# Kernel optimization log

Measured on AMD Instinct MI355X. Metric: run time of the kernel, lower is better.

Reference implementation:

```python
import jax, jax.numpy as jnp
import numpy as np

N_NODES = 10000
N_EDGES = 640000
NF = 128
HID = 128
NORM_FACTOR = 100.0


def setup_inputs() -> dict:
    key = jax.random.key(0)
    ks = jax.random.split(key, 8)
    s = lambda fan_in: 1.0 / np.sqrt(fan_in)
    return {
        "h": jax.random.normal(ks[0], (N_NODES, NF), dtype=jnp.float32),
        "edge_index": jax.random.randint(ks[1], (2, N_EDGES), 0, N_NODES, dtype=jnp.int64),
        "ew1": jax.random.normal(ks[2], (2 * NF, HID), dtype=jnp.float32) * s(2 * NF),
        "eb1": jnp.zeros((HID,), dtype=jnp.float32),
        "ew2": jax.random.normal(ks[3], (HID, HID), dtype=jnp.float32) * s(HID),
        "eb2": jnp.zeros((HID,), dtype=jnp.float32),
        "nw1": jax.random.normal(ks[4], (HID + NF, HID), dtype=jnp.float32) * s(HID + NF),
        "nb1": jnp.zeros((HID,), dtype=jnp.float32),
        "nw2": jax.random.normal(ks[5], (HID, NF), dtype=jnp.float32) * s(HID),
        "nb2": jnp.zeros((NF,), dtype=jnp.float32),
    }


def reference(h, edge_index, ew1, eb1, ew2, eb2, nw1, nb1, nw2, nb2):
    row, col = edge_index[0], edge_index[1]
    # edge model: gather endpoints, concat, 2-layer SiLU MLP -> mij [E, HID]
    x = jnp.concatenate([h[row], h[col]], axis=1)          # [E, 2*NF]
    mij = jax.nn.silu(x @ ew1 + eb1)
    mij = jax.nn.silu(mij @ ew2 + eb2)                     # [E, HID]
    # aggregation: scatter-add messages to source nodes, 'sum' normalization
    agg = jax.ops.segment_sum(mij, row, num_segments=h.shape[0]) / NORM_FACTOR
    # node model: residual MLP update
    a = jnp.concatenate([h, agg], axis=1)                  # [V, NF+HID]
    out = h + (jax.nn.silu(a @ nw1 + nb1) @ nw2 + nb2)     # [V, NF]
    return out, mij
```

## Files before the change

### kernel.cpp

```cpp
#include <hip/hip_runtime.h>

typedef __attribute__((ext_vector_type(8))) short short8;
typedef __attribute__((ext_vector_type(4))) float f32x4;
typedef unsigned short ushort_t;
typedef unsigned int uint_t;

#define MFMA16(a, b, c) __builtin_amdgcn_mfma_f32_16x16x32_bf16((a), (b), (c), 0, 0, 0)

constexpr int V = 10000;
constexpr int E = 640000;

__device__ __forceinline__ ushort_t f2b(float f) {
    uint_t u = __float_as_uint(f);
    u += 0x7FFFu + ((u >> 16) & 1u);
    return (ushort_t)(u >> 16);
}

__device__ __forceinline__ float silu(float x) {
    return x / (1.0f + __expf(-x));
}

__device__ __forceinline__ uint_t cvt_pk_bf16(float lo, float hi) {
    uint_t r;
    asm("v_cvt_pk_bf16_f32 %0, %1, %2" : "=v"(r) : "v"(lo), "v"(hi));
    return r;
}

__device__ __forceinline__ void wg_barrier_lds() {
    asm volatile("s_waitcnt lgkmcnt(0)" ::: "memory");
    __builtin_amdgcn_s_barrier();
    asm volatile("" ::: "memory");
}

__global__ void prep(const float* __restrict__ h,
                     const float* __restrict__ ew1, const float* __restrict__ ew2,
                     const float* __restrict__ nw1, const float* __restrict__ nw2,
                     ushort_t* __restrict__ hb,
                     ushort_t* __restrict__ w1T, ushort_t* __restrict__ w2T,
                     ushort_t* __restrict__ nw1T, ushort_t* __restrict__ nw2T,
                     float* __restrict__ agg) {
    int i = blockIdx.x * blockDim.x + threadIdx.x;
    if (i < V * 128) { hb[i] = f2b(h[i]); return; }
    i -= V * 128;
    if (i < V * 128) { agg[i] = 0.0f; return; }
    i -= V * 128;
    if (i < 256 * 128) { int k = i >> 7, c = i & 127; w1T[c * 256 + k] = f2b(ew1[i]); return; }
    i -= 256 * 128;
    if (i < 128 * 128) { int k = i >> 7, c = i & 127; w2T[c * 128 + k] = f2b(ew2[i]); return; }
    i -= 128 * 128;
    if (i < 256 * 128) { int k = i >> 7, c = i & 127; nw1T[c * 256 + k] = f2b(nw1[i]); return; }
    i -= 256 * 128;
    if (i < 128 * 128) { int k = i >> 7, c = i & 127; nw2T[c * 128 + k] = f2b(nw2[i]); }
}

__global__ __launch_bounds__(256, 2) void edge_kernel(
    const ushort_t* __restrict__ hb, const int* __restrict__ eidx,
    const ushort_t* __restrict__ w1, const float* __restrict__ eb1,
    const ushort_t* __restrict__ w2, const float* __restrict__ eb2,
    float* __restrict__ mij, float* __restrict__ agg) {
    __shared__ __align__(16) ushort_t xs[64 * 256];
    __shared__ __align__(16) ushort_t ys[64 * 128];
    __shared__ int ridx[2][64];

    const int tid = threadIdx.x;
    const int wave = tid >> 6;
    const int lane = tid & 63;
    const int quad = lane >> 4;
    const int ln = lane & 15;
    const int ncol0 = wave * 32;

    short8 b1f[8][2];
    short8 b2f[4][2];
#pragma unroll
    for (int kk = 0; kk < 8; kk++)
#pragma unroll
        for (int t = 0; t < 2; t++)
            b1f[kk][t] = *(const short8*)(w1 + (ncol0 + t * 16 + ln) * 256 + kk * 32 + quad * 8);
#pragma unroll
    for (int kk = 0; kk < 4; kk++)
#pragma unroll
        for (int t = 0; t < 2; t++)
            b2f[kk][t] = *(const short8*)(w2 + (ncol0 + t * 16 + ln) * 128 + kk * 32 + quad * 8);
    const float bv1[2] = {eb1[ncol0 + ln], eb1[ncol0 + 16 + ln]};
    const float bv2[2] = {eb2[ncol0 + ln], eb2[ncol0 + 16 + ln]};

    const int NT = E / 64;
    const int e = lane;
    const int seg = wave;
    char* const xrow = (char*)xs + e * 512;
    const int xswz = (e & 7) << 4;

    int tile = blockIdx.x;

    {
        const int r = eidx[tile * 64 + e];
        const int c = eidx[E + tile * 64 + e];
        if (seg == 0) ridx[0][e] = r;
        const int node = (seg < 2) ? r : c;
        const uint4* src = (const uint4*)(hb + node * 128 + (seg & 1) * 64);
#pragma unroll
        for (int u = 0; u < 8; u++)
            *(uint4*)(xrow + ((seg * 128 + u * 16) ^ xswz)) = src[u];
    }
    wg_barrier_lds();

    int p = 0;
    for (; tile < NT; tile += gridDim.x) {
        const int e0 = tile * 64;
        int tn = tile + gridDim.x;
        if (tn >= NT) tn = tile;

        const int rn = eidx[tn * 64 + e];
        const int cn = eidx[E + tn * 64 + e];
        const int noden = (seg < 2) ? rn : cn;
        const uint4* srcn = (const uint4*)(hb + noden * 128 + (seg & 1) * 64);
        uint4 st[8];
#pragma unroll
        for (int u = 0; u < 8; u++) st[u] = srcn[u];

        f32x4 acc[4][2];
#pragma unroll
        for (int mt = 0; mt < 4; mt++)
#pragma unroll
            for (int t = 0; t < 2; t++) acc[mt][t] = f32x4{bv1[t], bv1[t], bv1[t], bv1[t]};
#pragma unroll
        for (int kk = 0; kk < 8; kk++)
#pragma unroll
            for (int mt = 0; mt < 4; mt++) {
                const int row = mt * 16 + ln;
                short8 a = *(const short8*)((char*)xs + row * 512 +
                                            ((kk * 64 + quad * 16) ^ ((ln & 7) << 4)));
                acc[mt][0] = MFMA16(a, b1f[kk][0], acc[mt][0]);
                acc[mt][1] = MFMA16(a, b1f[kk][1], acc[mt][1]);
            }
#pragma unroll
        for (int mt = 0; mt < 4; mt++)
#pragma unroll
            for (int r4 = 0; r4 < 4; r4++) {
                const int row = mt * 16 + quad * 4 + r4;
                const uint_t pk = cvt_pk_bf16(silu(acc[mt][0][r4]), silu(acc[mt][1][r4]));
                char* yrow = (char*)ys + row * 256;
                const int ysw = (row & 7) << 4;
                const int cb = 2 * (ncol0 + ln);
                *(ushort_t*)(yrow + (cb ^ ysw)) = (ushort_t)pk;
                *(ushort_t*)(yrow + ((cb + 32) ^ ysw)) = (ushort_t)(pk >> 16);
            }
        wg_barrier_lds();

        if (seg == 0) ridx[p ^ 1][e] = rn;
#pragma unroll
        for (int u = 0; u < 8; u++)
            *(uint4*)(xrow + ((seg * 128 + u * 16) ^ xswz)) = st[u];

        f32x4 acc2[4][2];
#pragma unroll
        for (int mt = 0; mt < 4; mt++)
#pragma unroll
            for (int t = 0; t < 2; t++) acc2[mt][t] = f32x4{bv2[t], bv2[t], bv2[t], bv2[t]};
#pragma unroll
        for (int kk = 0; kk < 4; kk++)
#pragma unroll
            for (int mt = 0; mt < 4; mt++) {
                const int row = mt * 16 + ln;
                short8 a = *(const short8*)((char*)ys + row * 256 +
                                            ((kk * 64 + quad * 16) ^ ((ln & 7) << 4)));
                acc2[mt][0] = MFMA16(a, b2f[kk][0], acc2[mt][0]);
                acc2[mt][1] = MFMA16(a, b2f[kk][1], acc2[mt][1]);
            }

#pragma unroll
        for (int mt = 0; mt < 4; mt++)
#pragma unroll
            for (int r4 = 0; r4 < 4; r4++) {
                const int row = mt * 16 + quad * 4 + r4;
                const int nsrc = ridx[p][row];
#pragma unroll
                for (int t = 0; t < 2; t++) {
                    const float s = silu(acc2[mt][t][r4]);
                    const int col = ncol0 + t * 16 + ln;
                    mij[(size_t)(e0 + row) * 128 + col] = s;
                    unsafeAtomicAdd(&agg[nsrc * 128 + col], s);
                }
            }
        wg_barrier_lds();
        p ^= 1;
    }
}

__global__ __launch_bounds__(256, 2) void node_kernel(
    const ushort_t* __restrict__ hb, const float* __restrict__ h32,
    const float* __restrict__ agg,
    const ushort_t* __restrict__ w1, const float* __restrict__ nb1,
    const ushort_t* __restrict__ w2, const float* __restrict__ nb2,
    float* __restrict__ out) {
    __shared__ __align__(16) ushort_t xs[64 * 256];
    __shared__ __align__(16) ushort_t ys[64 * 128];

    const int tid = threadIdx.x;
    const int wave = tid >> 6;
    const int lane = tid & 63;
    const int quad = lane >> 4;
    const int ln = lane & 15;
    const int ncol0 = wave * 32;
    const int i0 = blockIdx.x * 64;

    short8 b1f[8][2];
    short8 b2f[4][2];
#pragma unroll
    for (int kk = 0; kk < 8; kk++)
#pragma unroll
        for (int t = 0; t < 2; t++)
            b1f[kk][t] = *(const short8*)(w1 + (ncol0 + t * 16 + ln) * 256 + kk * 32 + quad * 8);
#pragma unroll
    for (int kk = 0; kk < 4; kk++)
#pragma unroll
        for (int t = 0; t < 2; t++)
            b2f[kk][t] = *(const short8*)(w2 + (ncol0 + t * 16 + ln) * 128 + kk * 32 + quad * 8);
    const float bv1[2] = {nb1[ncol0 + ln], nb1[ncol0 + 16 + ln]};
    const float bv2[2] = {nb2[ncol0 + ln], nb2[ncol0 + 16 + ln]};

    const int e = lane, seg = wave;
    char* const xrow = (char*)xs + e * 512;
    const int xswz = (e & 7) << 4;
    const int node = i0 + e;

    if (node < V) {
        if (seg < 2) {
            const uint4* src = (const uint4*)(hb + node * 128 + seg * 64);
#pragma unroll
            for (int u = 0; u < 8; u++)
                *(uint4*)(xrow + ((seg * 128 + u * 16) ^ xswz)) = src[u];
        } else {
            const float4* src = (const float4*)(agg + node * 128 + (seg & 1) * 64);
#pragma unroll
            for (int u = 0; u < 8; u++) {
                float4 a = src[2 * u], b = src[2 * u + 1];
                uint4 v;
                v.x = cvt_pk_bf16(a.x * 0.01f, a.y * 0.01f);
                v.y = cvt_pk_bf16(a.z * 0.01f, a.w * 0.01f);
                v.z = cvt_pk_bf16(b.x * 0.01f, b.y * 0.01f);
                v.w = cvt_pk_bf16(b.z * 0.01f, b.w * 0.01f);
                *(uint4*)(xrow + ((seg * 128 + u * 16) ^ xswz)) = v;
            }
        }
    } else {
        const uint4 z{0, 0, 0, 0};
#pragma unroll
        for (int u = 0; u < 8; u++)
            *(uint4*)(xrow + ((seg * 128 + u * 16) ^ xswz)) = z;
    }
    __syncthreads();

    f32x4 acc[4][2];
#pragma unroll
    for (int mt = 0; mt < 4; mt++)
#pragma unroll
        for (int t = 0; t < 2; t++) acc[mt][t] = f32x4{bv1[t], bv1[t], bv1[t], bv1[t]};
#pragma unroll
    for (int kk = 0; kk < 8; kk++)
#pragma unroll
        for (int mt = 0; mt < 4; mt++) {
            const int row = mt * 16 + ln;
            short8 a = *(const short8*)((char*)xs + row * 512 +
                                        ((kk * 64 + quad * 16) ^ ((ln & 7) << 4)));
            acc[mt][0] = MFMA16(a, b1f[kk][0], acc[mt][0]);
            acc[mt][1] = MFMA16(a, b1f[kk][1], acc[mt][1]);
        }
#pragma unroll
    for (int mt = 0; mt < 4; mt++)
#pragma unroll
        for (int r4 = 0; r4 < 4; r4++) {
            const int row = mt * 16 + quad * 4 + r4;
            const uint_t pk = cvt_pk_bf16(silu(acc[mt][0][r4]), silu(acc[mt][1][r4]));
            char* yrow = (char*)ys + row * 256;
            const int ysw = (row & 7) << 4;
            const int cb = 2 * (ncol0 + ln);
            *(ushort_t*)(yrow + (cb ^ ysw)) = (ushort_t)pk;
            *(ushort_t*)(yrow + ((cb + 32) ^ ysw)) = (ushort_t)(pk >> 16);
        }
    __syncthreads();

    f32x4 acc2[4][2];
#pragma unroll
    for (int mt = 0; mt < 4; mt++)
#pragma unroll
        for (int t = 0; t < 2; t++) acc2[mt][t] = f32x4{bv2[t], bv2[t], bv2[t], bv2[t]};
#pragma unroll
    for (int kk = 0; kk < 4; kk++)
#pragma unroll
        for (int mt = 0; mt < 4; mt++) {
            const int row = mt * 16 + ln;
            short8 a = *(const short8*)((char*)ys + row * 256 +
                                        ((kk * 64 + quad * 16) ^ ((ln & 7) << 4)));
            acc2[mt][0] = MFMA16(a, b2f[kk][0], acc2[mt][0]);
            acc2[mt][1] = MFMA16(a, b2f[kk][1], acc2[mt][1]);
        }
#pragma unroll
    for (int mt = 0; mt < 4; mt++)
#pragma unroll
        for (int r4 = 0; r4 < 4; r4++) {
            const int row = mt * 16 + quad * 4 + r4;
            const int nd = i0 + row;
            if (nd < V) {
#pragma unroll
                for (int t = 0; t < 2; t++) {
                    const int col = ncol0 + t * 16 + ln;
                    out[(size_t)nd * 128 + col] = h32[(size_t)nd * 128 + col] + acc2[mt][t][r4];
                }
            }
        }
}

extern "C" void kernel_launch(void* const* d_in, const int* in_sizes, int n_in,
                              void* d_out, int out_size, void* d_ws, size_t ws_size,
                              hipStream_t stream) {
    const float* h = (const float*)d_in[0];
    const int* eidx = (const int*)d_in[1];
    const float* ew1 = (const float*)d_in[2];
    const float* eb1 = (const float*)d_in[3];
    const float* ew2 = (const float*)d_in[4];
    const float* eb2 = (const float*)d_in[5];
    const float* nw1 = (const float*)d_in[6];
    const float* nb1 = (const float*)d_in[7];
    const float* nw2 = (const float*)d_in[8];
    const float* nb2 = (const float*)d_in[9];

    float* out = (float*)d_out;
    float* mij = (float*)d_out + (size_t)V * 128;

    uint8_t* ws = (uint8_t*)d_ws;
    ushort_t* hb = (ushort_t*)(ws);
    ushort_t* w1b = (ushort_t*)(ws + 2560000);
    ushort_t* w2b = (ushort_t*)(ws + 2560000 + 65536);
    ushort_t* nw1b = (ushort_t*)(ws + 2560000 + 98304);
    ushort_t* nw2b = (ushort_t*)(ws + 2560000 + 163840);
    float* agg = (float*)(ws + 2560000 + 196608);

    constexpr int PREP_N = V * 128 + V * 128 + 256 * 128 + 128 * 128 + 256 * 128 + 128 * 128;
    prep<<<(PREP_N + 255) / 256, 256, 0, stream>>>(h, ew1, ew2, nw1, nw2,
                                                   hb, w1b, w2b, nw1b, nw2b, agg);

    edge_kernel<<<2000, 256, 0, stream>>>(hb, eidx, w1b, eb1, w2b, eb2, mij, agg);
    node_kernel<<<(V + 63) / 64, 256, 0, stream>>>(hb, h, agg, nw1b, nb1, nw2b, nb2, out);
}
```

Before: 604.5 us.

## Sort edges by source node and segment-reduce messages before atomics

Adds a counting sort (histogram, single-block scan, scatter) that builds a permutation of edges grouped by source node. The edge kernel processes edges in that order, writes mij at the original edge index, and sums each run of equal source nodes within the tile using ballot and shuffles. Each run then issues one atomic per column instead of one per edge. This targets the heavy global atomic traffic on agg, at the cost of extra preprocessing kernels, indirect index loads and a per-segment masked reduction loop.

```diff
diff --git a/kernel.cpp b/kernel.cpp
--- a/kernel.cpp
+++ b/kernel.cpp
@@ -38,7 +38,7 @@
                      ushort_t* __restrict__ hb,
                      ushort_t* __restrict__ w1T, ushort_t* __restrict__ w2T,
                      ushort_t* __restrict__ nw1T, ushort_t* __restrict__ nw2T,
-                     float* __restrict__ agg) {
+                     float* __restrict__ agg, int* __restrict__ cnt) {
     int i = blockIdx.x * blockDim.x + threadIdx.x;
     if (i < V * 128) { hb[i] = f2b(h[i]); return; }
     i -= V * 128;
@@ -50,17 +50,65 @@
     i -= 128 * 128;
     if (i < 256 * 128) { int k = i >> 7, c = i & 127; nw1T[c * 256 + k] = f2b(nw1[i]); return; }
     i -= 256 * 128;
-    if (i < 128 * 128) { int k = i >> 7, c = i & 127; nw2T[c * 128 + k] = f2b(nw2[i]); }
+    if (i < 128 * 128) { int k = i >> 7, c = i & 127; nw2T[c * 128 + k] = f2b(nw2[i]); return; }
+    i -= 128 * 128;
+    if (i < V) cnt[i] = 0;
+}
+
+__global__ void hist_kernel(const int* __restrict__ eidx, int* __restrict__ cnt) {
+    int e = blockIdx.x * blockDim.x + threadIdx.x;
+    if (e < E) atomicAdd(&cnt[eidx[e]], 1);
+}
+
+__global__ __launch_bounds__(256) void scan_kernel(const int* __restrict__ cnt,
+                                                   int* __restrict__ cursor) {
+    __shared__ int part[256];
+    const int t = threadIdx.x;
+    const int base = t * 40;
+    int s = 0;
+#pragma unroll 1
+    for (int i = 0; i < 40; i++) {
+        int idx = base + i;
+        s += (idx < V) ? cnt[idx] : 0;
+    }
+    part[t] = s;
+    __syncthreads();
+    for (int off = 1; off < 256; off <<= 1) {
+        int v = (t >= off) ? part[t - off] : 0;
+        __syncthreads();
+        part[t] += v;
+        __syncthreads();
+    }
+    int run = (t == 0) ? 0 : part[t - 1];
+#pragma unroll 1
+    for (int i = 0; i < 40; i++) {
+        int idx = base + i;
+        if (idx < V) {
+            cursor[idx] = run;
+            run += cnt[idx];
+        }
+    }
+}
+
+__global__ void scatter_kernel(const int* __restrict__ eidx, int* __restrict__ cursor,
+                               int* __restrict__ perm) {
+    int e = blockIdx.x * blockDim.x + threadIdx.x;
+    if (e < E) {
+        int pos = atomicAdd(&cursor[eidx[e]], 1);
+        perm[pos] = e;
+    }
 }
 
 __global__ __launch_bounds__(256, 2) void edge_kernel(
     const ushort_t* __restrict__ hb, const int* __restrict__ eidx,
+    const int* __restrict__ perm,
     const ushort_t* __restrict__ w1, const float* __restrict__ eb1,
     const ushort_t* __restrict__ w2, const float* __restrict__ eb2,
     float* __restrict__ mij, float* __restrict__ agg) {
     __shared__ __align__(16) ushort_t xs[64 * 256];
     __shared__ __align__(16) ushort_t ys[64 * 128];
     __shared__ int ridx[2][64];
+    __shared__ int pidx[2][64];
 
     const int tid = threadIdx.x;
     const int wave = tid >> 6;
@@ -68,6 +116,7 @@
     const int quad = lane >> 4;
     const int ln = lane & 15;
     const int ncol0 = wave * 32;
+    const int lnswz = (ln & 7) << 4;
 
     short8 b1f[8][2];
     short8 b2f[4][2];
@@ -85,6 +134,7 @@
     const float bv2[2] = {eb2[ncol0 + ln], eb2[ncol0 + 16 + ln]};
 
     const int NT = E / 64;
+    const int G = gridDim.x;
     const int e = lane;
     const int seg = wave;
     char* const xrow = (char*)xs + e * 512;
@@ -93,30 +143,34 @@
     int tile = blockIdx.x;
 
     {
-        const int r = eidx[tile * 64 + e];
-        const int c = eidx[E + tile * 64 + e];
-        if (seg == 0) ridx[0][e] = r;
+        const int pe = perm[tile * 64 + e];
+        const int r = eidx[pe];
+        const int c = eidx[E + pe];
+        if (seg == 0) { ridx[0][e] = r; pidx[0][e] = pe; }
         const int node = (seg < 2) ? r : c;
         const uint4* src = (const uint4*)(hb + node * 128 + (seg & 1) * 64);
 #pragma unroll
         for (int u = 0; u < 8; u++)
             *(uint4*)(xrow + ((seg * 128 + u * 16) ^ xswz)) = src[u];
     }
+    int t1 = tile + G; if (t1 >= NT) t1 = tile;
+    int pe1 = perm[t1 * 64 + e];
+    int r1 = eidx[pe1];
+    int c1 = eidx[E + pe1];
     wg_barrier_lds();
 
     int p = 0;
-    for (; tile < NT; tile += gridDim.x) {
-        const int e0 = tile * 64;
-        int tn = tile + gridDim.x;
-        if (tn >= NT) tn = tile;
-
-        const int rn = eidx[tn * 64 + e];
-        const int cn = eidx[E + tn * 64 + e];
-        const int noden = (seg < 2) ? rn : cn;
+    for (; tile < NT; tile += G) {
+        const int noden = (seg < 2) ? r1 : c1;
         const uint4* srcn = (const uint4*)(hb + noden * 128 + (seg & 1) * 64);
         uint4 st[8];
 #pragma unroll
         for (int u = 0; u < 8; u++) st[u] = srcn[u];
+
+        int t2 = tile + 2 * G; if (t2 >= NT) t2 = tile;
+        const int pe2 = perm[t2 * 64 + e];
+        const int r2 = eidx[pe2];
+        const int c2 = eidx[E + pe2];
 
         f32x4 acc[4][2];
 #pragma unroll
@@ -129,7 +183,7 @@
             for (int mt = 0; mt < 4; mt++) {
                 const int row = mt * 16 + ln;
                 short8 a = *(const short8*)((char*)xs + row * 512 +
-                                            ((kk * 64 + quad * 16) ^ ((ln & 7) << 4)));
+                                            ((kk * 64 + quad * 16) ^ lnswz));
                 acc[mt][0] = MFMA16(a, b1f[kk][0], acc[mt][0]);
                 acc[mt][1] = MFMA16(a, b1f[kk][1], acc[mt][1]);
             }
@@ -147,7 +201,7 @@
             }
         wg_barrier_lds();
 
-        if (seg == 0) ridx[p ^ 1][e] = rn;
+        if (seg == 0) { ridx[p ^ 1][e] = r1; pidx[p ^ 1][e] = pe1; }
 #pragma unroll
         for (int u = 0; u < 8; u++)
             *(uint4*)(xrow + ((seg * 128 + u * 16) ^ xswz)) = st[u];
@@ -163,7 +217,7 @@
             for (int mt = 0; mt < 4; mt++) {
                 const int row = mt * 16 + ln;
                 short8 a = *(const short8*)((char*)ys + row * 256 +
-                                            ((kk * 64 + quad * 16) ^ ((ln & 7) << 4)));
+                                            ((kk * 64 + quad * 16) ^ lnswz));
                 acc2[mt][0] = MFMA16(a, b2f[kk][0], acc2[mt][0]);
                 acc2[mt][1] = MFMA16(a, b2f[kk][1], acc2[mt][1]);
             }
@@ -173,16 +227,46 @@
 #pragma unroll
             for (int r4 = 0; r4 < 4; r4++) {
                 const int row = mt * 16 + quad * 4 + r4;
-                const int nsrc = ridx[p][row];
+                const int pe = pidx[p][row];
 #pragma unroll
                 for (int t = 0; t < 2; t++) {
                     const float s = silu(acc2[mt][t][r4]);
-                    const int col = ncol0 + t * 16 + ln;
-                    mij[(size_t)(e0 + row) * 128 + col] = s;
-                    unsafeAtomicAdd(&agg[nsrc * 128 + col], s);
+                    acc2[mt][t][r4] = s;
+                    mij[(size_t)pe * 128 + ncol0 + t * 16 + ln] = s;
                 }
             }
+
+        {
+            const int myn = ridx[p][lane];
+            const int prevn = (lane == 0) ? (myn + 1) : ridx[p][lane - 1];
+            unsigned long long bmask = __ballot(lane == 0 || myn != prevn);
+            while (bmask) {
+                const int a = __builtin_ctzll(bmask);
+                bmask &= bmask - 1;
+                const int b = bmask ? __builtin_ctzll(bmask) : 64;
+                float s0 = 0.0f, s1 = 0.0f;
+#pragma unroll
+                for (int mt = 0; mt < 4; mt++)
+#pragma unroll
+                    for (int r4 = 0; r4 < 4; r4++) {
+                        const int row = mt * 16 + quad * 4 + r4;
+                        const bool in = (row >= a) && (row < b);
+                        s0 += in ? acc2[mt][0][r4] : 0.0f;
+                        s1 += in ? acc2[mt][1][r4] : 0.0f;
+                    }
+                s0 += __shfl_xor(s0, 16);
+                s0 += __shfl_xor(s0, 32);
+                s1 += __shfl_xor(s1, 16);
+                s1 += __shfl_xor(s1, 32);
+                if (quad == 0) {
+                    const int node = ridx[p][a];
+                    unsafeAtomicAdd(&agg[node * 128 + ncol0 + ln], s0);
+                    unsafeAtomicAdd(&agg[node * 128 + ncol0 + 16 + ln], s1);
+                }
+            }
+        }
         wg_barrier_lds();
+        pe1 = pe2; r1 = r2; c1 = c2;
         p ^= 1;
     }
 }
@@ -203,6 +287,7 @@
     const int ln = lane & 15;
     const int ncol0 = wave * 32;
     const int i0 = blockIdx.x * 64;
+    const int lnswz = (ln & 7) << 4;
 
     short8 b1f[8][2];
     short8 b2f[4][2];
@@ -262,7 +347,7 @@
         for (int mt = 0; mt < 4; mt++) {
             const int row = mt * 16 + ln;
             short8 a = *(const short8*)((char*)xs + row * 512 +
-                                        ((kk * 64 + quad * 16) ^ ((ln & 7) << 4)));
+                                        ((kk * 64 + quad * 16) ^ lnswz));
             acc[mt][0] = MFMA16(a, b1f[kk][0], acc[mt][0]);
             acc[mt][1] = MFMA16(a, b1f[kk][1], acc[mt][1]);
         }
@@ -291,7 +376,7 @@
         for (int mt = 0; mt < 4; mt++) {
             const int row = mt * 16 + ln;
             short8 a = *(const short8*)((char*)ys + row * 256 +
-                                        ((kk * 64 + quad * 16) ^ ((ln & 7) << 4)));
+                                        ((kk * 64 + quad * 16) ^ lnswz));
             acc2[mt][0] = MFMA16(a, b2f[kk][0], acc2[mt][0]);
             acc2[mt][1] = MFMA16(a, b2f[kk][1], acc2[mt][1]);
         }
@@ -334,12 +419,19 @@
     ushort_t* w2b = (ushort_t*)(ws + 2560000 + 65536);
     ushort_t* nw1b = (ushort_t*)(ws + 2560000 + 98304);
     ushort_t* nw2b = (ushort_t*)(ws + 2560000 + 163840);
-    float* agg = (float*)(ws + 2560000 + 196608);
-
-    constexpr int PREP_N = V * 128 + V * 128 + 256 * 128 + 128 * 128 + 256 * 128 + 128 * 128;
+    float* agg = (float*)(ws + 2756608);
+    int* cnt = (int*)(ws + 7876608);
+    int* perm = (int*)(ws + 7916608);
+    int* cursor = (int*)(ws + 10476608);
+
+    constexpr int PREP_N =
+        V * 128 + V * 128 + 256 * 128 + 128 * 128 + 256 * 128 + 128 * 128 + V;
     prep<<<(PREP_N + 255) / 256, 256, 0, stream>>>(h, ew1, ew2, nw1, nw2,
-                                                   hb, w1b, w2b, nw1b, nw2b, agg);
-
-    edge_kernel<<<2000, 256, 0, stream>>>(hb, eidx, w1b, eb1, w2b, eb2, mij, agg);
+                                                   hb, w1b, w2b, nw1b, nw2b, agg, cnt);
+    hist_kernel<<<(E + 255) / 256, 256, 0, stream>>>(eidx, cnt);
+    scan_kernel<<<1, 256, 0, stream>>>(cnt, cursor);
+    scatter_kernel<<<(E + 255) / 256, 256, 0, stream>>>(eidx, cursor, perm);
+
+    edge_kernel<<<2000, 256, 0, stream>>>(hb, eidx, perm, w1b, eb1, w2b, eb2, mij, agg);
     node_kernel<<<(V + 63) / 64, 256, 0, stream>>>(hb, h, agg, nw1b, nb1, nw2b, nb2, out);
 }
```

Result: no change. 602.4 us (-0.4%).
